# Kernel tuning notes

Measured on AMD Instinct MI355X. Metric: run time of the kernel, lower is better.

## Reference

```python
import jax, jax.numpy as jnp
import numpy as np

D_MODEL = 1024
HIDDEN = 64


def setup_inputs() -> dict:
    key = jax.random.key(0)
    ks = jax.random.split(key, 11)
    B, N = 8, 4096
    scale_in = 1.0 / np.sqrt(D_MODEL)
    scale_h = 1.0 / np.sqrt(HIDDEN)
    return {
        "query": jax.random.normal(ks[0], (B, N, D_MODEL), jnp.float32),
        "key": jax.random.normal(ks[1], (B, N, D_MODEL), jnp.float32),
        "value": jax.random.normal(ks[2], (B, N, D_MODEL), jnp.float32),
        # torch nn.Linear(d_model, 64): weight [64, d_model], bias [64]
        "Wq": jax.random.uniform(ks[3], (HIDDEN, D_MODEL), jnp.float32, -scale_in, scale_in),
        "bq": jax.random.uniform(ks[4], (HIDDEN,), jnp.float32, -scale_in, scale_in),
        "Wk": jax.random.uniform(ks[5], (HIDDEN, D_MODEL), jnp.float32, -scale_in, scale_in),
        "bk": jax.random.uniform(ks[6], (HIDDEN,), jnp.float32, -scale_in, scale_in),
        "Wv": jax.random.uniform(ks[7], (HIDDEN, D_MODEL), jnp.float32, -scale_in, scale_in),
        "bv": jax.random.uniform(ks[8], (HIDDEN,), jnp.float32, -scale_in, scale_in),
        # project: nn.Linear(64, d_model): weight [d_model, 64], bias [d_model]
        "Wp": jax.random.uniform(ks[9], (D_MODEL, HIDDEN), jnp.float32, -scale_h, scale_h),
        "bp": jax.random.uniform(ks[10], (D_MODEL,), jnp.float32, -scale_h, scale_h),
    }


def reference(query, key, value, Wq, bq, Wk, bk, Wv, bv, Wp, bp):
    # q/k/v projections: [B, N, d_model] -> [B, N, 64]
    q = jnp.einsum('bnd,hd->bnh', query, Wq) + bq
    k = jnp.einsum('bnd,hd->bnh', key, Wk) + bk
    v = jnp.einsum('bnd,hd->bnh', value, Wv) + bv
    # softmax over sequence dim (dim=1), weighted pool over sequence -> [B, 1, 64]
    attn = jax.nn.softmax(k, axis=1)
    weights = jnp.sum(attn * v, axis=1, keepdims=True)
    # gated broadcast: sigmoid(q) * pooled weights -> [B, N, 64]
    Yt = jax.nn.sigmoid(q) * weights
    # project back: [B, N, 64] -> [B, N, d_model]
    return jnp.einsum('bnh,dh->bnd', Yt, Wp) + bp
```

## Files before the change

### kernel.cpp

```cpp
#include <hip/hip_runtime.h>
#include <hip/hip_bf16.h>

#define BB 8
#define NN 4096
#define DD 1024
#define HH 64

typedef __bf16 bf8v __attribute__((ext_vector_type(8)));
typedef __bf16 bf4v __attribute__((ext_vector_type(4)));
typedef float  f4v  __attribute__((ext_vector_type(4)));
typedef __hip_bfloat16 bf16;

__device__ __forceinline__ f4v mfma16x16x32(bf8v a, bf8v b, f4v c) {
    return __builtin_amdgcn_mfma_f32_16x16x32_bf16(a, b, c, 0, 0, 0);
}

__device__ __forceinline__ bf8v pack8(f4v a, f4v b) {
    bf8v r;
    #pragma unroll
    for (int i = 0; i < 4; ++i) { r[i] = (__bf16)a[i]; r[i + 4] = (__bf16)b[i]; }
    return r;
}

__device__ __forceinline__ bf8v ldg8(const bf16* p) { return *(const bf8v*)p; }

__device__ __forceinline__ void gload_lds16(const float* g, float* l) {
    __builtin_amdgcn_global_load_lds(
        (const __attribute__((address_space(1))) void*)g,
        (__attribute__((address_space(3))) void*)l,
        16, 0, 0);
}

__global__ __launch_bounds__(256) void convert_weights_kernel(
    const float* __restrict__ Wq, const float* __restrict__ Wk,
    const float* __restrict__ Wv, const float* __restrict__ Wp,
    bf16* __restrict__ cw)
{
    const int idx = blockIdx.x * 256 + threadIdx.x;
    const int t = idx >> 14;
    const int e = (idx & 16383) * 4;
    const float* src = (t == 0) ? Wq : (t == 1) ? Wk : (t == 2) ? Wv : Wp;
    f4v x = *(const f4v*)(src + e);
    bf4v r;
    #pragma unroll
    for (int i = 0; i < 4; ++i) r[i] = (__bf16)x[i];
    *(bf4v*)(cw + t * 65536 + e) = r;
}

__global__ __launch_bounds__(256, 4) void proj_kernel(
    const float* __restrict__ query, const float* __restrict__ key,
    const float* __restrict__ value, const bf16* __restrict__ cw,
    const float* __restrict__ bq, const float* __restrict__ bk,
    const float* __restrict__ bv,
    float* __restrict__ se, float* __restrict__ sev,
    float* __restrict__ gate)
{
    __shared__ __align__(16) float As0[2][4][512];
    __shared__ __align__(16) float As1[2][4][512];

    const int lane = threadIdx.x & 63;
    const int wave = threadIdx.x >> 6;
    const int cl   = lane & 15;
    const int quad = lane >> 4;

    const int is_q = blockIdx.x >> 9;
    const int bid  = blockIdx.x & 511;
    const int b     = bid >> 6;
    const int chunk = bid & 63;
    const int row0  = chunk * 64 + wave * 16;

    const int sr = lane >> 3;
    const int sc = (lane & 7) ^ sr;
    const size_t soff0 = ((size_t)b * NN + row0 + sr) * DD + sc * 4;
    const size_t soff1 = soff0 + (size_t)8 * DD;

    const int sw  = cl & 7;
    const int flo = cl * 32 + ((((quad * 2)    ) ^ sw) << 2);
    const int fhi = cl * 32 + ((((quad * 2) + 1) ^ sw) << 2);

    if (!is_q) {
        const float* kb = key   + soff0;
        const float* vb = value + soff0;
        const bf16* wkb = cw + 1 * 65536 + (size_t)cl * DD + quad * 8;
        const bf16* wvb = cw + 2 * 65536 + (size_t)cl * DD + quad * 8;

        f4v kacc[4], vacc[4];
        #pragma unroll
        for (int i = 0; i < 4; ++i) {
            kacc[i] = (f4v){0.f, 0.f, 0.f, 0.f};
            vacc[i] = (f4v){0.f, 0.f, 0.f, 0.f};
        }

        gload_lds16(kb,            &As0[0][wave][0]);
        gload_lds16(kb + 8 * DD,   &As0[0][wave][256]);
        gload_lds16(vb,            &As1[0][wave][0]);
        gload_lds16(vb + 8 * DD,   &As1[0][wave][256]);

        #pragma unroll 2
        for (int t = 0; t < 32; ++t) {
            asm volatile("s_waitcnt vmcnt(0) lgkmcnt(0)" ::: "memory");
            const int bb = t & 1;
            const float* ak = &As0[bb][wave][0];
            const float* av = &As1[bb][wave][0];
            f4v klo = *(const f4v*)(ak + flo);
            f4v khi = *(const f4v*)(ak + fhi);
            f4v vlo = *(const f4v*)(av + flo);
            f4v vhi = *(const f4v*)(av + fhi);

            const int k0 = t * 32;
            bf8v wk8[4], wv8[4];
            #pragma unroll
            for (int ht = 0; ht < 4; ++ht) {
                wk8[ht] = ldg8(wkb + (size_t)ht * 16 * DD + k0);
                wv8[ht] = ldg8(wvb + (size_t)ht * 16 * DD + k0);
            }

            if (t < 31) {
                const int nb = bb ^ 1;
                const int kn = (t + 1) * 32;
                gload_lds16(kb + kn,          &As0[nb][wave][0]);
                gload_lds16(kb + 8 * DD + kn, &As0[nb][wave][256]);
                gload_lds16(vb + kn,          &As1[nb][wave][0]);
                gload_lds16(vb + 8 * DD + kn, &As1[nb][wave][256]);
            }

            bf8v akf = pack8(klo, khi);
            bf8v avf = pack8(vlo, vhi);
            #pragma unroll
            for (int ht = 0; ht < 4; ++ht) {
                kacc[ht] = mfma16x16x32(akf, wk8[ht], kacc[ht]);
                vacc[ht] = mfma16x16x32(avf, wv8[ht], vacc[ht]);
            }
        }

        #pragma unroll
        for (int ht = 0; ht < 4; ++ht) {
            const int h = ht * 16 + cl;
            const float bkh = bk[h];
            const float bvh = bv[h];
            float sep = 0.f, sevp = 0.f;
            #pragma unroll
            for (int r = 0; r < 4; ++r) {
                float e = __expf(kacc[ht][r] + bkh);
                sep  += e;
                sevp += e * (vacc[ht][r] + bvh);
            }
            sep  += __shfl_xor(sep, 16, 64);
            sevp += __shfl_xor(sevp, 16, 64);
            sep  += __shfl_xor(sep, 32, 64);
            sevp += __shfl_xor(sevp, 32, 64);
            if (quad == 0) {
                atomicAdd(&se[b * HH + h], sep);
                atomicAdd(&sev[b * HH + h], sevp);
            }
        }
    } else {
        const float* qb = query + soff0;
        const bf16* wqb = cw + (size_t)cl * DD + quad * 8;

        f4v qacc[4];
        #pragma unroll
        for (int i = 0; i < 4; ++i) qacc[i] = (f4v){0.f, 0.f, 0.f, 0.f};

        gload_lds16(qb,          &As0[0][wave][0]);
        gload_lds16(qb + 8 * DD, &As0[0][wave][256]);

        #pragma unroll 2
        for (int t = 0; t < 32; ++t) {
            asm volatile("s_waitcnt vmcnt(0) lgkmcnt(0)" ::: "memory");
            const int bb = t & 1;
            const float* aq = &As0[bb][wave][0];
            f4v qlo = *(const f4v*)(aq + flo);
            f4v qhi = *(const f4v*)(aq + fhi);

            const int k0 = t * 32;
            bf8v wq8[4];
            #pragma unroll
            for (int ht = 0; ht < 4; ++ht)
                wq8[ht] = ldg8(wqb + (size_t)ht * 16 * DD + k0);

            if (t < 31) {
                const int nb = bb ^ 1;
                const int kn = (t + 1) * 32;
                gload_lds16(qb + kn,          &As0[nb][wave][0]);
                gload_lds16(qb + 8 * DD + kn, &As0[nb][wave][256]);
            }

            bf8v aqf = pack8(qlo, qhi);
            #pragma unroll
            for (int ht = 0; ht < 4; ++ht)
                qacc[ht] = mfma16x16x32(aqf, wq8[ht], qacc[ht]);
        }

        const size_t gbase = ((size_t)b * NN + row0 + quad * 4) * HH;
        #pragma unroll
        for (int ht = 0; ht < 4; ++ht) {
            const int h = ht * 16 + cl;
            const float bqh = bq[h];
            #pragma unroll
            for (int r = 0; r < 4; ++r) {
                float qv = qacc[ht][r] + bqh;
                float sg = 1.0f / (1.0f + __expf(-qv));
                gate[gbase + (size_t)r * HH + h] = sg;
            }
        }
    }
}

__global__ __launch_bounds__(256) void out_kernel(
    const float* __restrict__ gate, const bf16* __restrict__ cWp,
    const float* __restrict__ bp, const float* __restrict__ se,
    const float* __restrict__ sev, float* __restrict__ out)
{
    const int lane = threadIdx.x & 63;
    const int wave = threadIdx.x >> 6;
    const int cl   = lane & 15;
    const int quad = lane >> 4;
    const int b     = blockIdx.x >> 8;
    const int chunk = blockIdx.x & 255;
    const int row0  = chunk * 16;

    const float* gp = gate + ((size_t)b * NN + row0 + cl) * HH + quad * 8;

    bf8v a2[2];
    #pragma unroll
    for (int kk = 0; kk < 2; ++kk) {
        f4v g0 = *(const f4v*)(gp + kk * 32);
        f4v g1 = *(const f4v*)(gp + kk * 32 + 4);
        const int hb = kk * 32 + quad * 8;
        f4v s0 = *(const f4v*)(se  + b * HH + hb);
        f4v s1 = *(const f4v*)(se  + b * HH + hb + 4);
        f4v v0 = *(const f4v*)(sev + b * HH + hb);
        f4v v1 = *(const f4v*)(sev + b * HH + hb + 4);
        #pragma unroll
        for (int j = 0; j < 4; ++j) {
            a2[kk][j]     = (__bf16)(g0[j] * __fdividef(v0[j], s0[j]));
            a2[kk][j + 4] = (__bf16)(g1[j] * __fdividef(v1[j], s1[j]));
        }
    }

    const bf16* wp = cWp + (size_t)cl * HH + quad * 8;
    const size_t outbase = ((size_t)b * NN + row0 + quad * 4) * DD;

    #pragma unroll 4
    for (int nt = 0; nt < 16; ++nt) {
        const int d0 = wave * 256 + nt * 16;
        f4v o = (f4v){0.f, 0.f, 0.f, 0.f};
        o = mfma16x16x32(a2[0], ldg8(wp + (size_t)d0 * HH), o);
        o = mfma16x16x32(a2[1], ldg8(wp + (size_t)d0 * HH + 32), o);
        const int dcol = d0 + cl;
        const float bpd = bp[dcol];
        #pragma unroll
        for (int r = 0; r < 4; ++r)
            out[outbase + (size_t)r * DD + dcol] = o[r] + bpd;
    }
}

extern "C" void kernel_launch(void* const* d_in, const int* in_sizes, int n_in,
                              void* d_out, int out_size, void* d_ws, size_t ws_size,
                              hipStream_t stream)
{
    const float* query = (const float*)d_in[0];
    const float* key_  = (const float*)d_in[1];
    const float* value = (const float*)d_in[2];
    const float* Wq = (const float*)d_in[3];
    const float* bq = (const float*)d_in[4];
    const float* Wk = (const float*)d_in[5];
    const float* bk = (const float*)d_in[6];
    const float* Wv = (const float*)d_in[7];
    const float* bv = (const float*)d_in[8];
    const float* Wp = (const float*)d_in[9];
    const float* bp = (const float*)d_in[10];
    float* out = (float*)d_out;

    float* se   = (float*)d_ws;
    float* sev  = se + BB * HH;
    bf16*  cw   = (bf16*)((char*)d_ws + 4096);
    float* gate = (float*)((char*)d_ws + 4096 + 4 * 65536 * sizeof(bf16));

    hipMemsetAsync(d_ws, 0, 2 * BB * HH * sizeof(float), stream);

    convert_weights_kernel<<<dim3(256), dim3(256), 0, stream>>>(Wq, Wk, Wv, Wp, cw);
    proj_kernel<<<dim3(1024), dim3(256), 0, stream>>>(
        query, key_, value, cw, bq, bk, bv, se, sev, gate);
    out_kernel<<<dim3(2048), dim3(256), 0, stream>>>(
        gate, cw + 3 * 65536, bp, se, sev, out);
}
```

Before: 484.8 us.

## Triple-buffer LDS activation tiles and prefetch weights one step ahead in projection

The projection kernel moves from double to triple buffering of its LDS activation tiles, issuing async loads two steps ahead. The bf16 weight fragments are now loaded into registers one iteration early. The full vmcnt(0)/lgkmcnt(0) drain each step is replaced by partial vmcnt waits, with sched_barriers to pin the issue order. The larger LDS footprint lowers the launch-bounds occupancy hint from 4 to 3, which may cut latency hiding from parallel waves.

New measurement: 483.1 us. No clear change (-0.3%).

```diff
diff --git a/kernel.cpp b/kernel.cpp
--- a/kernel.cpp
+++ b/kernel.cpp
@@ -10,6 +10,8 @@
 typedef __bf16 bf4v __attribute__((ext_vector_type(4)));
 typedef float  f4v  __attribute__((ext_vector_type(4)));
 typedef __hip_bfloat16 bf16;
+
+#define SB0() __builtin_amdgcn_sched_barrier(0)
 
 __device__ __forceinline__ f4v mfma16x16x32(bf8v a, bf8v b, f4v c) {
     return __builtin_amdgcn_mfma_f32_16x16x32_bf16(a, b, c, 0, 0, 0);
@@ -47,7 +49,7 @@
     *(bf4v*)(cw + t * 65536 + e) = r;
 }
 
-__global__ __launch_bounds__(256, 4) void proj_kernel(
+__global__ __launch_bounds__(256, 3) void proj_kernel(
     const float* __restrict__ query, const float* __restrict__ key,
     const float* __restrict__ value, const bf16* __restrict__ cw,
     const float* __restrict__ bq, const float* __restrict__ bk,
@@ -55,8 +57,8 @@
     float* __restrict__ se, float* __restrict__ sev,
     float* __restrict__ gate)
 {
-    __shared__ __align__(16) float As0[2][4][512];
-    __shared__ __align__(16) float As1[2][4][512];
+    __shared__ __align__(16) float As0[3][4][512];
+    __shared__ __align__(16) float As1[3][4][512];
 
     const int lane = threadIdx.x & 63;
     const int wave = threadIdx.x >> 6;
@@ -72,7 +74,6 @@
     const int sr = lane >> 3;
     const int sc = (lane & 7) ^ sr;
     const size_t soff0 = ((size_t)b * NN + row0 + sr) * DD + sc * 4;
-    const size_t soff1 = soff0 + (size_t)8 * DD;
 
     const int sw  = cl & 7;
     const int flo = cl * 32 + ((((quad * 2)    ) ^ sw) << 2);
@@ -91,45 +92,61 @@
             vacc[i] = (f4v){0.f, 0.f, 0.f, 0.f};
         }
 
-        gload_lds16(kb,            &As0[0][wave][0]);
-        gload_lds16(kb + 8 * DD,   &As0[0][wave][256]);
-        gload_lds16(vb,            &As1[0][wave][0]);
-        gload_lds16(vb + 8 * DD,   &As1[0][wave][256]);
-
-        #pragma unroll 2
+        bf8v wk8[2][4], wv8[2][4];
+
+        gload_lds16(kb,          &As0[0][wave][0]);
+        gload_lds16(kb + 8 * DD, &As0[0][wave][256]);
+        gload_lds16(vb,          &As1[0][wave][0]);
+        gload_lds16(vb + 8 * DD, &As1[0][wave][256]);
+        SB0();
+        #pragma unroll
+        for (int ht = 0; ht < 4; ++ht) {
+            wk8[0][ht] = ldg8(wkb + (size_t)ht * 16 * DD);
+            wv8[0][ht] = ldg8(wvb + (size_t)ht * 16 * DD);
+        }
+        SB0();
+        gload_lds16(kb + 32,          &As0[1][wave][0]);
+        gload_lds16(kb + 8 * DD + 32, &As0[1][wave][256]);
+        gload_lds16(vb + 32,          &As1[1][wave][0]);
+        gload_lds16(vb + 8 * DD + 32, &As1[1][wave][256]);
+
+        #pragma unroll
         for (int t = 0; t < 32; ++t) {
-            asm volatile("s_waitcnt vmcnt(0) lgkmcnt(0)" ::: "memory");
-            const int bb = t & 1;
-            const float* ak = &As0[bb][wave][0];
-            const float* av = &As1[bb][wave][0];
+            if (t < 31) { asm volatile("s_waitcnt vmcnt(12)" ::: "memory"); }
+            else        { asm volatile("s_waitcnt vmcnt(8)"  ::: "memory"); }
+            SB0();
+            const int st = t % 3;
+            const float* ak = &As0[st][wave][0];
+            const float* av = &As1[st][wave][0];
             f4v klo = *(const f4v*)(ak + flo);
             f4v khi = *(const f4v*)(ak + fhi);
             f4v vlo = *(const f4v*)(av + flo);
             f4v vhi = *(const f4v*)(av + fhi);
-
-            const int k0 = t * 32;
-            bf8v wk8[4], wv8[4];
+            bf8v akf = pack8(klo, khi);
+            bf8v avf = pack8(vlo, vhi);
+
+            const int cb = t & 1, nb = cb ^ 1;
             #pragma unroll
             for (int ht = 0; ht < 4; ++ht) {
-                wk8[ht] = ldg8(wkb + (size_t)ht * 16 * DD + k0);
-                wv8[ht] = ldg8(wvb + (size_t)ht * 16 * DD + k0);
+                kacc[ht] = mfma16x16x32(akf, wk8[cb][ht], kacc[ht]);
+                vacc[ht] = mfma16x16x32(avf, wv8[cb][ht], vacc[ht]);
             }
 
             if (t < 31) {
-                const int nb = bb ^ 1;
-                const int kn = (t + 1) * 32;
-                gload_lds16(kb + kn,          &As0[nb][wave][0]);
-                gload_lds16(kb + 8 * DD + kn, &As0[nb][wave][256]);
-                gload_lds16(vb + kn,          &As1[nb][wave][0]);
-                gload_lds16(vb + 8 * DD + kn, &As1[nb][wave][256]);
-            }
-
-            bf8v akf = pack8(klo, khi);
-            bf8v avf = pack8(vlo, vhi);
-            #pragma unroll
-            for (int ht = 0; ht < 4; ++ht) {
-                kacc[ht] = mfma16x16x32(akf, wk8[ht], kacc[ht]);
-                vacc[ht] = mfma16x16x32(avf, wv8[ht], vacc[ht]);
+                const int k0 = (t + 1) * 32;
+                #pragma unroll
+                for (int ht = 0; ht < 4; ++ht) {
+                    wk8[nb][ht] = ldg8(wkb + (size_t)ht * 16 * DD + k0);
+                    wv8[nb][ht] = ldg8(wvb + (size_t)ht * 16 * DD + k0);
+                }
+            }
+            if (t < 30) {
+                const int kn = (t + 2) * 32;
+                const int sn = (t + 2) % 3;
+                gload_lds16(kb + kn,          &As0[sn][wave][0]);
+                gload_lds16(kb + 8 * DD + kn, &As0[sn][wave][256]);
+                gload_lds16(vb + kn,          &As1[sn][wave][0]);
+                gload_lds16(vb + 8 * DD + kn, &As1[sn][wave][256]);
             }
         }
 
@@ -162,34 +179,46 @@
         #pragma unroll
         for (int i = 0; i < 4; ++i) qacc[i] = (f4v){0.f, 0.f, 0.f, 0.f};
 
+        bf8v wq8[2][4];
+
         gload_lds16(qb,          &As0[0][wave][0]);
         gload_lds16(qb + 8 * DD, &As0[0][wave][256]);
-
-        #pragma unroll 2
+        SB0();
+        #pragma unroll
+        for (int ht = 0; ht < 4; ++ht)
+            wq8[0][ht] = ldg8(wqb + (size_t)ht * 16 * DD);
+        SB0();
+        gload_lds16(qb + 32,          &As0[1][wave][0]);
+        gload_lds16(qb + 8 * DD + 32, &As0[1][wave][256]);
+
+        #pragma unroll
         for (int t = 0; t < 32; ++t) {
-            asm volatile("s_waitcnt vmcnt(0) lgkmcnt(0)" ::: "memory");
-            const int bb = t & 1;
-            const float* aq = &As0[bb][wave][0];
+            if (t < 31) { asm volatile("s_waitcnt vmcnt(10)" ::: "memory"); }
+            else        { asm volatile("s_waitcnt vmcnt(8)"  ::: "memory"); }
+            SB0();
+            const int st = t % 3;
+            const float* aq = &As0[st][wave][0];
             f4v qlo = *(const f4v*)(aq + flo);
             f4v qhi = *(const f4v*)(aq + fhi);
-
-            const int k0 = t * 32;
-            bf8v wq8[4];
+            bf8v aqf = pack8(qlo, qhi);
+
+            const int cb = t & 1, nb = cb ^ 1;
             #pragma unroll
             for (int ht = 0; ht < 4; ++ht)
-                wq8[ht] = ldg8(wqb + (size_t)ht * 16 * DD + k0);
+                qacc[ht] = mfma16x16x32(aqf, wq8[cb][ht], qacc[ht]);
 
             if (t < 31) {
-                const int nb = bb ^ 1;
-                const int kn = (t + 1) * 32;
-                gload_lds16(qb + kn,          &As0[nb][wave][0]);
-                gload_lds16(qb + 8 * DD + kn, &As0[nb][wave][256]);
-            }
-
-            bf8v aqf = pack8(qlo, qhi);
-            #pragma unroll
-            for (int ht = 0; ht < 4; ++ht)
-                qacc[ht] = mfma16x16x32(aqf, wq8[ht], qacc[ht]);
+                const int k0 = (t + 1) * 32;
+                #pragma unroll
+                for (int ht = 0; ht < 4; ++ht)
+                    wq8[nb][ht] = ldg8(wqb + (size_t)ht * 16 * DD + k0);
+            }
+            if (t < 30) {
+                const int kn = (t + 2) * 32;
+                const int sn = (t + 2) % 3;
+                gload_lds16(qb + kn,          &As0[sn][wave][0]);
+                gload_lds16(qb + 8 * DD + kn, &As0[sn][wave][256]);
+            }
         }
 
         const size_t gbase = ((size_t)b * NN + row0 + quad * 4) * HH;
```
